# Kernel tuning notes

Hardware: AMD Instinct MI355X
Metric: run time of the kernel (lower is better)

The kernel has to match this reference:

```python
import jax, jax.numpy as jnp
import numpy as np

BS, D, S, K = 32, 64, 2048, 1024  # batch, embedding_dim, seq_len, num_embeddings


def setup_inputs() -> dict:
    key = jax.random.key(0)
    k1, k2 = jax.random.split(key)
    x = jax.random.normal(k1, (BS, D, S), dtype=jnp.float32)
    # xavier_uniform on [D, K]
    bound = float(np.sqrt(6.0 / (D + K)))
    embeddings = jax.random.uniform(k2, (D, K), dtype=jnp.float32, minval=-bound, maxval=bound)
    return {"x": x, "embeddings": embeddings}


def reference(x, embeddings):
    bs, d, s = x.shape
    k = embeddings.shape[1]
    # [bs, d, s] -> [bs*s, d]
    flat = x.transpose(0, 2, 1).reshape(-1, d)
    unquantized = flat
    # squared distance ||a||^2 - 2 a.b + ||b||^2 -> [N, K]
    a2 = jnp.sum(flat * flat, axis=1, keepdims=True)
    ab2 = 2.0 * (flat @ embeddings)
    b2 = jnp.sum(embeddings * embeddings, axis=0, keepdims=True)
    distance = a2 - ab2 + b2
    encoding_indices = jnp.argmin(distance, axis=1)  # == (-distance).argmax(1)
    one_hot = jax.nn.one_hot(encoding_indices, k, dtype=jnp.int32)  # F.one_hot -> int
    quantized = jnp.take(embeddings.T, encoding_indices, axis=0)  # [N, d] gather
    quantized = quantized.reshape(bs, s, d).transpose(0, 2, 1)  # [bs, d, s]
    e_latent_loss = jnp.mean(jnp.square(quantized - jax.lax.stop_gradient(x)))
    q_latent_loss = jnp.mean(jnp.square(jax.lax.stop_gradient(quantized) - x))
    loss = q_latent_loss + e_latent_loss
    # straight-through estimator
    quantized_st = x + jax.lax.stop_gradient(quantized - x)
    return (
        quantized_st,
        loss,
        one_hot.reshape(bs, s, k).transpose(0, 2, 1),
        encoding_indices.reshape(bs, s),
        distance.reshape(bs, s, k).transpose(0, 2, 1),
        unquantized,
        embeddings.T,
    )
```

## Files before the change

### kernel.cpp

```cpp
#include <hip/hip_runtime.h>

typedef float f32x16 __attribute__((ext_vector_type(16)));

#define BSZ 32
#define DIM 64
#define SEQ 2048
#define KE  1024

#define O0 0ull
#define O1 4194304ull
#define O2 4194305ull
#define O3 71303169ull
#define O4 71368705ull
#define O5 138477569ull
#define O6 142671873ull

__global__ __launch_bounds__(256) void vq_prep(const float* __restrict__ E,
                                               float* __restrict__ out,
                                               float* __restrict__ et_ws,
                                               float* __restrict__ b2_ws) {
    __shared__ float T[64][65];
    const int tid  = threadIdx.x;
    const int lane = tid & 63;
    const int sub  = tid >> 6;
    const int k0   = blockIdx.x * 64;
    for (int dd = 0; dd < 16; ++dd) {
        int d = dd * 4 + sub;
        T[d][lane] = E[(size_t)d * KE + k0 + lane];
    }
    __syncthreads();
    for (int ii = 0; ii < 16; ++ii) {
        int kl = ii * 4 + sub;
        float v = T[lane][kl];
        out[O6 + (size_t)(k0 + kl) * 64 + lane] = v;
        et_ws[(size_t)(k0 + kl) * 64 + lane]    = v;
    }
    if (tid < 64) {
        float s = 0.f;
        #pragma unroll
        for (int d = 0; d < 64; ++d) {
            float v = T[d][tid];
            s = fmaf(v, v, s);
        }
        b2_ws[k0 + tid] = s;
    }
    if (blockIdx.x == 0 && tid == 0) out[O1] = 0.f;
}

__global__ __launch_bounds__(256, 4) void vq_main(const float* __restrict__ x,
                                                  const float* __restrict__ et,
                                                  const float* __restrict__ b2,
                                                  float* __restrict__ out) {
    __shared__ float mD[4][64];
    __shared__ int   mK[4][64];
    __shared__ int   idxs[64];

    const int tid  = threadIdx.x;
    const int lane = tid & 63;
    const int wv   = __builtin_amdgcn_readfirstlane(tid >> 6);
    const int b    = blockIdx.x >> 5;
    const int s0   = (blockIdx.x & 31) << 6;
    const int s    = s0 + lane;

    const float* xp = x + ((size_t)b << 17) + s;
    float xr[64];
    #pragma unroll
    for (int d = 0; d < 64; ++d) xr[d] = xp[(size_t)d << 11];
    float a2 = 0.f;
    #pragma unroll
    for (int d = 0; d < 64; ++d) a2 = fmaf(xr[d], xr[d], a2);

    float bestD = 3.4e38f;
    int   bestK = wv << 8;
    float* outD = out + O4 + ((size_t)b << 21) + s;

    const int kbase = wv << 8;
    #pragma unroll 1
    for (int kk = 0; kk < 256; ++kk) {
        const int k = kbase + kk;
        const float* ep = et + ((size_t)k << 6);
        f32x16 e0, e1, e2, e3;
        float  bb;
        asm volatile("s_load_dwordx16 %0, %1, 0x0"  : "=s"(e0) : "s"(ep));
        asm volatile("s_load_dwordx16 %0, %1, 0x40" : "=s"(e1) : "s"(ep));
        asm volatile("s_load_dwordx16 %0, %1, 0x80" : "=s"(e2) : "s"(ep));
        asm volatile("s_load_dwordx16 %0, %1, 0xc0" : "=s"(e3) : "s"(ep));
        asm volatile("s_load_dword %0, %1, 0x0"     : "=s"(bb) : "s"(b2 + k));
        asm volatile("s_waitcnt lgkmcnt(0)"
                     : "+s"(e0), "+s"(e1), "+s"(e2), "+s"(e3), "+s"(bb));
        float d0 = 0.f, d1 = 0.f, d2 = 0.f, d3 = 0.f;
        #pragma unroll
        for (int j = 0; j < 16; ++j) {
            d0 = fmaf(xr[j],      e0[j], d0);
            d1 = fmaf(xr[16 + j], e1[j], d1);
            d2 = fmaf(xr[32 + j], e2[j], d2);
            d3 = fmaf(xr[48 + j], e3[j], d3);
        }
        float dist = fmaf(-2.f, (d0 + d1) + (d2 + d3), a2 + bb);
        outD[(size_t)k << 11] = dist;
        if (dist < bestD) { bestD = dist; bestK = k; }
    }

    mD[wv][lane] = bestD;
    mK[wv][lane] = bestK;
    __syncthreads();
    if (tid < 64) {
        float bD = mD[0][tid]; int bK = mK[0][tid];
        #pragma unroll
        for (int w = 1; w < 4; ++w) {
            float dw = mD[w][tid]; int kw = mK[w][tid];
            if (dw < bD || (dw == bD && kw < bK)) { bD = dw; bK = kw; }
        }
        idxs[tid] = bK;
        out[O3 + (size_t)b * SEQ + s0 + tid] = (float)bK;
    }
    __syncthreads();
    const int myidx = idxs[lane];

    float* outH = out + O2 + ((size_t)b << 21) + s0 + lane;
    for (int i = 0; i < 256; ++i) {
        int k = (i << 2) + wv;
        outH[(size_t)k << 11] = (k == myidx) ? 1.f : 0.f;
    }

    if (wv == 0) {
        const float* q = et + ((size_t)myidx << 6);
        float* outQ = out + O0 + ((size_t)b << 17) + s;
        float lsum = 0.f;
        #pragma unroll
        for (int d = 0; d < 64; ++d) {
            float qv = q[d];
            outQ[(size_t)d << 11] = qv;
            float df = qv - xr[d];
            lsum = fmaf(df, df, lsum);
        }
        #pragma unroll
        for (int m = 32; m >= 1; m >>= 1) lsum += __shfl_xor(lsum, m, 64);
        if (lane == 0) atomicAdd(out + O1, lsum * (2.f / 4194304.f));
    }
}

__global__ __launch_bounds__(256) void vq_unq(const float* __restrict__ x,
                                              float* __restrict__ out) {
    __shared__ float T[64][65];
    const int tid  = threadIdx.x;
    const int lane = tid & 63;
    const int sub  = tid >> 6;
    const int b    = blockIdx.x >> 5;
    const int s0   = (blockIdx.x & 31) << 6;
    const float* xp = x + ((size_t)b << 17) + s0;
    for (int dd = 0; dd < 16; ++dd) {
        int d = dd * 4 + sub;
        T[d][lane] = xp[((size_t)d << 11) + lane];
    }
    __syncthreads();
    float* op = out + O5 + (((size_t)b << 11) + s0) * 64;
    for (int ii = 0; ii < 16; ++ii) {
        int sl = ii * 4 + sub;
        op[(size_t)sl * 64 + lane] = T[lane][sl];
    }
}

extern "C" void kernel_launch(void* const* d_in, const int* in_sizes, int n_in,
                              void* d_out, int out_size, void* d_ws, size_t ws_size,
                              hipStream_t stream) {
    const float* x = (const float*)d_in[0];
    const float* E = (const float*)d_in[1];
    float* out   = (float*)d_out;
    float* et_ws = (float*)d_ws;
    float* b2_ws = et_ws + 65536;
    vq_prep<<<16, 256, 0, stream>>>(E, out, et_ws, b2_ws);
    vq_main<<<1024, 256, 0, stream>>>(x, et_ws, b2_ws, out);
    vq_unq<<<1024, 256, 0, stream>>>(x, out);
}
```

Before: 276.6 us.

## Pack codebook norms into padded rows, use vector loads, fuse one-hot zeroing

Each codebook row now has a stride of 68 floats, and its squared norm is stored at slot 64. The main loop reads rows with uniform float4 vector loads instead of inline-asm scalar loads and drops the readfirstlane, and the loop is unrolled by 2. The one-hot output is written as zeros inside the distance loop, and a single 1 is then scattered at the argmin, replacing the separate strided one-hot pass. This trades scalar-cache broadcast for per-lane vector loads of uniform addresses, which may add VMEM traffic, but it interleaves the one-hot stores with compute.

```diff
diff --git a/kernel.cpp b/kernel.cpp
--- a/kernel.cpp
+++ b/kernel.cpp
@@ -1,11 +1,10 @@
 #include <hip/hip_runtime.h>
-
-typedef float f32x16 __attribute__((ext_vector_type(16)));
 
 #define BSZ 32
 #define DIM 64
 #define SEQ 2048
 #define KE  1024
+#define ETS 68
 
 #define O0 0ull
 #define O1 4194304ull
@@ -17,8 +16,7 @@
 
 __global__ __launch_bounds__(256) void vq_prep(const float* __restrict__ E,
                                                float* __restrict__ out,
-                                               float* __restrict__ et_ws,
-                                               float* __restrict__ b2_ws) {
+                                               float* __restrict__ et_ws) {
     __shared__ float T[64][65];
     const int tid  = threadIdx.x;
     const int lane = tid & 63;
@@ -33,7 +31,7 @@
         int kl = ii * 4 + sub;
         float v = T[lane][kl];
         out[O6 + (size_t)(k0 + kl) * 64 + lane] = v;
-        et_ws[(size_t)(k0 + kl) * 64 + lane]    = v;
+        et_ws[(size_t)(k0 + kl) * ETS + lane]    = v;
     }
     if (tid < 64) {
         float s = 0.f;
@@ -42,14 +40,13 @@
             float v = T[d][tid];
             s = fmaf(v, v, s);
         }
-        b2_ws[k0 + tid] = s;
+        et_ws[(size_t)(k0 + tid) * ETS + 64] = s;
     }
     if (blockIdx.x == 0 && tid == 0) out[O1] = 0.f;
 }
 
 __global__ __launch_bounds__(256, 4) void vq_main(const float* __restrict__ x,
                                                   const float* __restrict__ et,
-                                                  const float* __restrict__ b2,
                                                   float* __restrict__ out) {
     __shared__ float mD[4][64];
     __shared__ int   mK[4][64];
@@ -57,7 +54,7 @@
 
     const int tid  = threadIdx.x;
     const int lane = tid & 63;
-    const int wv   = __builtin_amdgcn_readfirstlane(tid >> 6);
+    const int wv   = tid >> 6;
     const int b    = blockIdx.x >> 5;
     const int s0   = (blockIdx.x & 31) << 6;
     const int s    = s0 + lane;
@@ -71,33 +68,28 @@
     for (int d = 0; d < 64; ++d) a2 = fmaf(xr[d], xr[d], a2);
 
     float bestD = 3.4e38f;
-    int   bestK = wv << 8;
+    const int kbase = wv << 8;
+    int   bestK = kbase;
     float* outD = out + O4 + ((size_t)b << 21) + s;
+    float* outH = out + O2 + ((size_t)b << 21) + s;
 
-    const int kbase = wv << 8;
-    #pragma unroll 1
+    #pragma unroll 2
     for (int kk = 0; kk < 256; ++kk) {
         const int k = kbase + kk;
-        const float* ep = et + ((size_t)k << 6);
-        f32x16 e0, e1, e2, e3;
-        float  bb;
-        asm volatile("s_load_dwordx16 %0, %1, 0x0"  : "=s"(e0) : "s"(ep));
-        asm volatile("s_load_dwordx16 %0, %1, 0x40" : "=s"(e1) : "s"(ep));
-        asm volatile("s_load_dwordx16 %0, %1, 0x80" : "=s"(e2) : "s"(ep));
-        asm volatile("s_load_dwordx16 %0, %1, 0xc0" : "=s"(e3) : "s"(ep));
-        asm volatile("s_load_dword %0, %1, 0x0"     : "=s"(bb) : "s"(b2 + k));
-        asm volatile("s_waitcnt lgkmcnt(0)"
-                     : "+s"(e0), "+s"(e1), "+s"(e2), "+s"(e3), "+s"(bb));
+        const float4* ep = (const float4*)(et + (size_t)k * ETS);
+        float4 eb = ep[16];
         float d0 = 0.f, d1 = 0.f, d2 = 0.f, d3 = 0.f;
         #pragma unroll
-        for (int j = 0; j < 16; ++j) {
-            d0 = fmaf(xr[j],      e0[j], d0);
-            d1 = fmaf(xr[16 + j], e1[j], d1);
-            d2 = fmaf(xr[32 + j], e2[j], d2);
-            d3 = fmaf(xr[48 + j], e3[j], d3);
+        for (int g = 0; g < 16; ++g) {
+            float4 e = ep[g];
+            d0 = fmaf(xr[4*g+0], e.x, d0);
+            d1 = fmaf(xr[4*g+1], e.y, d1);
+            d2 = fmaf(xr[4*g+2], e.z, d2);
+            d3 = fmaf(xr[4*g+3], e.w, d3);
         }
-        float dist = fmaf(-2.f, (d0 + d1) + (d2 + d3), a2 + bb);
+        float dist = fmaf(-2.f, (d0 + d1) + (d2 + d3), a2 + eb.x);
         outD[(size_t)k << 11] = dist;
+        outH[(size_t)k << 11] = 0.f;
         if (dist < bestD) { bestD = dist; bestK = k; }
     }
 
@@ -113,18 +105,13 @@
         }
         idxs[tid] = bK;
         out[O3 + (size_t)b * SEQ + s0 + tid] = (float)bK;
+        out[O2 + ((size_t)b << 21) + ((size_t)bK << 11) + s0 + tid] = 1.f;
     }
     __syncthreads();
     const int myidx = idxs[lane];
 
-    float* outH = out + O2 + ((size_t)b << 21) + s0 + lane;
-    for (int i = 0; i < 256; ++i) {
-        int k = (i << 2) + wv;
-        outH[(size_t)k << 11] = (k == myidx) ? 1.f : 0.f;
-    }
-
     if (wv == 0) {
-        const float* q = et + ((size_t)myidx << 6);
+        const float* q = et + (size_t)myidx * ETS;
         float* outQ = out + O0 + ((size_t)b << 17) + s;
         float lsum = 0.f;
         #pragma unroll
@@ -168,8 +155,7 @@
     const float* E = (const float*)d_in[1];
     float* out   = (float*)d_out;
     float* et_ws = (float*)d_ws;
-    float* b2_ws = et_ws + 65536;
-    vq_prep<<<16, 256, 0, stream>>>(E, out, et_ws, b2_ws);
-    vq_main<<<1024, 256, 0, stream>>>(x, et_ws, b2_ws, out);
+    vq_prep<<<16, 256, 0, stream>>>(E, out, et_ws);
+    vq_main<<<1024, 256, 0, stream>>>(x, et_ws, out);
     vq_unq<<<1024, 256, 0, stream>>>(x, out);
 }
```

New measurement: 519.9 us. 1.88x slower.
